# Optimization experiments

Hardware: AMD Instinct MI355X
Metric: run time of the kernel (lower is better)

## Reference

```python
import jax, jax.numpy as jnp
import numpy as np

KSIZE = 7
CUBIC_A = -0.5


def cubic_contribution(x, a=CUBIC_A):
    ax = jnp.abs(x)
    ax2 = ax * ax
    ax3 = ax * ax2
    cont_01 = ((a + 2) * ax3 - (a + 3) * ax2 + 1) * (ax <= 1).astype(x.dtype)
    cont_12 = (a * ax3 - 5 * a * ax2 + 8 * a * ax - 4 * a) * jnp.logical_and(ax > 1, ax <= 2).astype(x.dtype)
    return cont_01 + cont_12


def projective_grid(H, W, m, eps_x=0.0, eps_y=0.0):
    # Apply 3x3 homography m to pixel centers (x+eps_x, y+eps_y); returns (2, H*W).
    xs = jnp.arange(W, dtype=jnp.float32) + eps_x
    ys = jnp.arange(H, dtype=jnp.float32) + eps_y
    yy, xx = jnp.meshgrid(ys, xs, indexing='ij')
    xx = xx.ravel()
    yy = yy.ravel()
    X = m[0, 0] * xx + m[0, 1] * yy + m[0, 2]
    Y = m[1, 0] * xx + m[1, 1] * yy + m[1, 2]
    Z = m[2, 0] * xx + m[2, 1] * yy + m[2, 2]
    return jnp.stack((X / Z, Y / Z))


def setup_inputs() -> dict:
    key = jax.random.key(0)
    k1, k2 = jax.random.split(key)
    H = W = 1024
    N = H * W
    # near-identity homography (avoids degenerate perspective divide)
    m_inverse = jnp.eye(3, dtype=jnp.float32) + 0.001 * jax.random.normal(k1, (3, 3), dtype=jnp.float32)
    # source-space sampling positions, in-image range
    grid = jax.random.uniform(k2, (2, N), dtype=jnp.float32) * jnp.array([[W - 1.0], [H - 1.0]], dtype=jnp.float32)
    yi = jnp.arange(N, dtype=jnp.int32)
    return {"m_inverse": m_inverse, "grid": grid, "H": H, "W": W, "yi": yi}


def reference(m_inverse, grid, H, W, yi):
    K = KSIZE
    pad = K // 2
    offset = (K % 2) / 2  # 0.5 for odd kernels

    pos = grid + 1 - offset                      # (2, N)
    pos_frac = pos - jnp.floor(pos)              # (2, N)

    pl = projective_grid(H, W, m_inverse, eps_x=-0.5)
    pr = projective_grid(H, W, m_inverse, eps_x=0.5)
    pt = projective_grid(H, W, m_inverse, eps_y=-0.5)
    pb = projective_grid(H, W, m_inverse, eps_y=0.5)

    du = (pb - pt)[:, yi][:, :, None, None]      # (2, N, 1, 1)
    dv = (pr - pl)[:, yi][:, :, None, None]      # (2, N, 1, 1)

    # regularize |du| >= 1
    len_du = jnp.sqrt(du[0] ** 2 + du[1] ** 2)   # (N, 1, 1)
    mask_du = len_du < 1.0
    du = jnp.where(mask_du[None], du / len_du[None], du)
    len_du = jnp.where(mask_du, 1.0, len_du)

    # regularize |dv| >= 1
    len_dv = jnp.sqrt(dv[0] ** 2 + dv[1] ** 2)
    mask_dv = len_dv < 1.0
    dv = jnp.where(mask_dv[None], dv / len_dv[None], dv)
    len_dv = jnp.where(mask_dv, 1.0, len_dv)

    det = du[0] * dv[1] - du[1] * dv[0]          # (N, 1, 1)
    len_du = len_du * det
    len_dv = len_dv * det

    pos_w = jnp.linspace(pad - K + 1, pad, K).astype(jnp.float32) + offset  # (K,)
    pw = pos_frac[:, :, None] - pos_w[None, None, :]                        # (2, N, K)
    pos_wx = pw[0][:, None, :]                   # (N, 1, K)
    pos_wy = pw[1][:, :, None]                   # (N, K, 1)

    pos_wxp = (dv[1] * pos_wx - du[1] * pos_wy) / len_du  # (N, K, K)
    pos_wyp = (du[0] * pos_wy - dv[0] * pos_wx) / len_dv  # (N, K, K)

    x = du[0] * pos_wxp + du[1] * pos_wyp        # (N, K, K)
    y = dv[0] * pos_wxp + dv[1] * pos_wyp        # (N, K, K)

    weight = (cubic_contribution(x) * cubic_contribution(y)).reshape(x.shape[0], -1)  # (N, K*K)
    weight = weight / jnp.sum(weight, axis=-1, keepdims=True)
    return weight
```

## Files before the change

### kernel.cpp

```cpp
#include <hip/hip_runtime.h>

#define K 7
#define KK 49
#define BLK 256
#define TPP 2
#define PPB (BLK / TPP)
#define NW 25
#define CHUNK_F4 (PPB * KK / 4)

__device__ __forceinline__ float cubic_c(float x) {
    float ax = __builtin_fabsf(x);
    float t2 = __builtin_fmaxf(2.0f - ax, 0.0f);
    float t1 = __builtin_fmaxf(1.0f - ax, 0.0f);
    float r  = (t2 * t2) * __builtin_fmaf(0.5f, t2, -0.5f);
    return __builtin_fmaf(t1 * t1, __builtin_fmaf(-2.0f, t1, 1.0f), r);
}

__global__ __launch_bounds__(BLK, 6) void kest_kernel(
    const float* __restrict__ m,
    const float* __restrict__ grid,
    const int*   __restrict__ Wp,
    const int*   __restrict__ yi,
    float*       __restrict__ out,
    int N)
{
    __shared__ __align__(16) float lds[PPB * KK];

    const int tid  = threadIdx.x;
    const int sub  = tid & (TPP - 1);
    const int pixL = tid >> 1;
    const int i    = blockIdx.x * PPB + pixL;

    if (i < N) {
        const float m00 = m[0], m01 = m[1], m02 = m[2];
        const float m10 = m[3], m11 = m[4], m12 = m[5];
        const float m20 = m[6], m21 = m[7], m22 = m[8];
        const int   W   = Wp[0];

        const int j = yi[i];
        int yyI, xxI;
        if ((W & (W - 1)) == 0) {
            yyI = j >> (__ffs(W) - 1);
            xxI = j & (W - 1);
        } else {
            yyI = j / W;
            xxI = j - yyI * W;
        }
        const float xx = (float)xxI;
        const float yy = (float)yyI;

        const float X0 = m00 * xx + m01 * yy + m02;
        const float Y0 = m10 * xx + m11 * yy + m12;
        const float Z0 = m20 * xx + m21 * yy + m22;

        const float izy = __builtin_amdgcn_rcpf(Z0 * Z0 - 0.25f * m21 * m21);
        float du0 = (m01 * Z0 - m21 * X0) * izy;
        float du1 = (m11 * Z0 - m21 * Y0) * izy;
        const float izx = __builtin_amdgcn_rcpf(Z0 * Z0 - 0.25f * m20 * m20);
        float dv0 = (m00 * Z0 - m20 * X0) * izx;
        float dv1 = (m10 * Z0 - m20 * Y0) * izx;

        const float d2u = du0 * du0 + du1 * du1;
        const float rlu = __builtin_amdgcn_rsqf(d2u);
        float len_du = d2u * rlu;
        if (len_du < 1.0f) { du0 *= rlu; du1 *= rlu; len_du = 1.0f; }
        const float d2v = dv0 * dv0 + dv1 * dv1;
        const float rlv = __builtin_amdgcn_rsqf(d2v);
        float len_dv = d2v * rlv;
        if (len_dv < 1.0f) { dv0 *= rlv; dv1 *= rlv; len_dv = 1.0f; }

        const float det  = du0 * dv1 - du1 * dv0;
        const float r_du = __builtin_amdgcn_rcpf(len_du * det);
        const float r_dv = __builtin_amdgcn_rcpf(len_dv * det);

        const float p1 = du0 * dv1, p2 = du1 * dv0;
        const float Axx = p1 * r_du - p2 * r_dv;
        const float Axy = du0 * du1 * (r_dv - r_du);
        const float Ayx = dv0 * dv1 * (r_du - r_dv);
        const float Ayy = p1 * r_dv - p2 * r_du;

        const float px  = grid[i]     + 0.5f;
        const float py  = grid[N + i] + 0.5f;
        const float fxc = (px - __builtin_floorf(px)) + 2.5f;
        const float fyc = (py - __builtin_floorf(py)) + 2.5f;
        const float subf = (float)sub;

        float wv[NW];
        float wsum = 0.0f;
#pragma unroll
        for (int qq = 0; qq < NW; ++qq) {
            const int c0 = (2 * qq) % 7,  c1 = (2 * qq + 1) % 7;
            const int r0 = (2 * qq) / 7,  r1 = (2 * qq + 1) / 7;
            const float wxv = __builtin_fmaf(subf, (float)(c0 - c1), fxc - (float)c0);
            const float wyv = __builtin_fmaf(subf, (float)(r0 - r1), fyc - (float)r0);
            const float x = __builtin_fmaf(Axx, wxv, Axy * wyv);
            const float y = __builtin_fmaf(Ayx, wxv, Ayy * wyv);
            float t = cubic_c(x) * cubic_c(y);
            if (qq == NW - 1) t = sub ? 0.0f : t;
            wv[qq] = t;
            wsum += t;
        }
        wsum += __shfl_xor(wsum, 1);
        const float rs = __builtin_amdgcn_rcpf(wsum);

        float* p = &lds[pixL * KK + sub];
#pragma unroll
        for (int qq = 0; qq < NW; ++qq) {
            if (qq < NW - 1 || sub == 0)
                p[2 * qq] = wv[qq] * rs;
        }
    }
    __syncthreads();

    const long long baseF4 = (long long)blockIdx.x * CHUNK_F4;
    const long long limF4  = ((long long)N * KK) >> 2;
    const float4* src = (const float4*)lds;
    float4*       dst = (float4*)out + baseF4;
#pragma unroll
    for (int k = 0; k < 7; ++k) {
        const int t = tid + k * BLK;
        if (t < CHUNK_F4 && baseF4 + t < limF4) dst[t] = src[t];
    }
}

extern "C" void kernel_launch(void* const* d_in, const int* in_sizes, int n_in,
                              void* d_out, int out_size, void* d_ws, size_t ws_size,
                              hipStream_t stream) {
    const float* m    = (const float*)d_in[0];
    const float* grid = (const float*)d_in[1];
    const int*   Wp   = (const int*)d_in[3];
    const int*   yi   = (const int*)d_in[4];
    float*       out  = (float*)d_out;
    const int N = in_sizes[4];

    const int blocks = (N + PPB - 1) / PPB;
    kest_kernel<<<blocks, BLK, 0, stream>>>(m, grid, Wp, yi, out, N);
}
```

Baseline: 219.8 us.

## Share per-pixel setup via shuffles, use packed float2 math, per-wave LDS staging

Only the first 32 lanes of each wavefront compute the per-pixel homography Jacobian and fractional offsets. The results are broadcast with shuffles to the two threads that handle each pixel, so the setup work is no longer done twice. The 49-tap cubic weight loop is rewritten with two-wide float vectors so the compiler can emit packed FP32 instructions. Each wavefront now stages and stores its own LDS slice, which removes the block-wide barrier, and a scalar tail path handles the partial last block. The costs are extra shuffle instructions and a reliance on intra-wave ordering of LDS writes and reads without an explicit barrier.

```diff
diff --git a/kernel.cpp b/kernel.cpp
--- a/kernel.cpp
+++ b/kernel.cpp
@@ -1,19 +1,23 @@
 #include <hip/hip_runtime.h>
 
-#define K 7
 #define KK 49
 #define BLK 256
-#define TPP 2
-#define PPB (BLK / TPP)
-#define NW 25
-#define CHUNK_F4 (PPB * KK / 4)
+#define PPW 32
+#define PPB 128
+#define WFL (PPW * KK)
+#define WF4 (WFL / 4)
 
-__device__ __forceinline__ float cubic_c(float x) {
-    float ax = __builtin_fabsf(x);
-    float t2 = __builtin_fmaxf(2.0f - ax, 0.0f);
-    float t1 = __builtin_fmaxf(1.0f - ax, 0.0f);
-    float r  = (t2 * t2) * __builtin_fmaf(0.5f, t2, -0.5f);
-    return __builtin_fmaf(t1 * t1, __builtin_fmaf(-2.0f, t1, 1.0f), r);
+typedef float v2f __attribute__((ext_vector_type(2)));
+
+static __device__ __forceinline__ v2f v2bc(float s) { v2f r; r.x = s; r.y = s; return r; }
+
+static __device__ __forceinline__ v2f cubic2(v2f x) {
+    v2f ax = __builtin_elementwise_abs(x);
+    v2f t2 = __builtin_elementwise_max(v2bc(2.0f) - ax, v2bc(0.0f));
+    v2f t1 = __builtin_elementwise_max(v2bc(1.0f) - ax, v2bc(0.0f));
+    v2f r  = (t2 * t2) * __builtin_elementwise_fma(v2bc(0.5f), t2, v2bc(-0.5f));
+    return __builtin_elementwise_fma(t1 * t1,
+              __builtin_elementwise_fma(v2bc(-2.0f), t1, v2bc(1.0f)), r);
 }
 
 __global__ __launch_bounds__(BLK, 6) void kest_kernel(
@@ -24,102 +28,145 @@
     float*       __restrict__ out,
     int N)
 {
-    __shared__ __align__(16) float lds[PPB * KK];
+    __shared__ __align__(16) float lds[4 * WFL];
 
-    const int tid  = threadIdx.x;
-    const int sub  = tid & (TPP - 1);
-    const int pixL = tid >> 1;
-    const int i    = blockIdx.x * PPB + pixL;
+    const int tid   = threadIdx.x;
+    const int wv_   = tid >> 6;
+    const int lane  = tid & 63;
+    const int pixW  = lane >> 1;
+    const int sub   = lane & 1;
+    const int blockBase = blockIdx.x * PPB;
+    float* ldsW = &lds[wv_ * WFL];
 
+    float Axx = 0.f, Axy = 0.f, Ayx = 0.f, Ayy = 0.f, fxc = 0.f, fyc = 0.f;
+    if (lane < 32) {
+        const int p = blockBase + wv_ * PPW + lane;
+        if (p < N) {
+            const float m00 = m[0], m01 = m[1], m02 = m[2];
+            const float m10 = m[3], m11 = m[4], m12 = m[5];
+            const float m20 = m[6], m21 = m[7], m22 = m[8];
+            const int   W   = Wp[0];
+
+            const int j = yi[p];
+            int yyI, xxI;
+            if ((W & (W - 1)) == 0) {
+                yyI = j >> (__ffs(W) - 1);
+                xxI = j & (W - 1);
+            } else {
+                yyI = j / W;
+                xxI = j - yyI * W;
+            }
+            const float xx = (float)xxI, yy = (float)yyI;
+
+            const float X0 = m00 * xx + m01 * yy + m02;
+            const float Y0 = m10 * xx + m11 * yy + m12;
+            const float Z0 = m20 * xx + m21 * yy + m22;
+
+            const float izy = __builtin_amdgcn_rcpf(Z0 * Z0 - 0.25f * m21 * m21);
+            float du0 = (m01 * Z0 - m21 * X0) * izy;
+            float du1 = (m11 * Z0 - m21 * Y0) * izy;
+            const float izx = __builtin_amdgcn_rcpf(Z0 * Z0 - 0.25f * m20 * m20);
+            float dv0 = (m00 * Z0 - m20 * X0) * izx;
+            float dv1 = (m10 * Z0 - m20 * Y0) * izx;
+
+            const float d2u = du0 * du0 + du1 * du1;
+            const float rlu = __builtin_amdgcn_rsqf(d2u);
+            float len_du = d2u * rlu;
+            if (len_du < 1.0f) { du0 *= rlu; du1 *= rlu; len_du = 1.0f; }
+            const float d2v = dv0 * dv0 + dv1 * dv1;
+            const float rlv = __builtin_amdgcn_rsqf(d2v);
+            float len_dv = d2v * rlv;
+            if (len_dv < 1.0f) { dv0 *= rlv; dv1 *= rlv; len_dv = 1.0f; }
+
+            const float det  = du0 * dv1 - du1 * dv0;
+            const float r_du = __builtin_amdgcn_rcpf(len_du * det);
+            const float r_dv = __builtin_amdgcn_rcpf(len_dv * det);
+
+            const float p1 = du0 * dv1, p2 = du1 * dv0;
+            Axx = p1 * r_du - p2 * r_dv;
+            Axy = du0 * du1 * (r_dv - r_du);
+            Ayx = dv0 * dv1 * (r_du - r_dv);
+            Ayy = p1 * r_dv - p2 * r_du;
+
+            const float px = grid[p]     + 0.5f;
+            const float py = grid[N + p] + 0.5f;
+            fxc = (px - __builtin_floorf(px)) + 2.5f;
+            fyc = (py - __builtin_floorf(py)) + 2.5f;
+        }
+    }
+    Axx = __shfl(Axx, pixW); Axy = __shfl(Axy, pixW);
+    Ayx = __shfl(Ayx, pixW); Ayy = __shfl(Ayy, pixW);
+    fxc = __shfl(fxc, pixW); fyc = __shfl(fyc, pixW);
+
+    const int i = blockBase + wv_ * PPW + pixW;
     if (i < N) {
-        const float m00 = m[0], m01 = m[1], m02 = m[2];
-        const float m10 = m[3], m11 = m[4], m12 = m[5];
-        const float m20 = m[6], m21 = m[7], m22 = m[8];
-        const int   W   = Wp[0];
+        const float subf = (float)sub;
+        const v2f subf2 = v2bc(subf);
+        const v2f Axx2 = v2bc(Axx), Axy2 = v2bc(Axy);
+        const v2f Ayx2 = v2bc(Ayx), Ayy2 = v2bc(Ayy);
 
-        const int j = yi[i];
-        int yyI, xxI;
-        if ((W & (W - 1)) == 0) {
-            yyI = j >> (__ffs(W) - 1);
-            xxI = j & (W - 1);
-        } else {
-            yyI = j / W;
-            xxI = j - yyI * W;
+        v2f wv2[13];
+        v2f ws2 = v2bc(0.0f);
+#pragma unroll
+        for (int j = 0; j < 13; ++j) {
+            const int q0 = 4 * j, q1 = 4 * j + 2;
+            const float cx0 = (float)(q0 % 7), cx1 = (float)(q1 % 7);
+            const float dx0 = (float)((q0 + 1) % 7 - q0 % 7);
+            const float dx1 = (float)((q1 + 1) % 7 - q1 % 7);
+            const float ry0 = (float)(q0 / 7), ry1 = (float)(q1 / 7);
+            const float dy0 = (float)((q0 + 1) / 7 - q0 / 7);
+            const float dy1 = (float)((q1 + 1) / 7 - q1 / 7);
+
+            v2f wxv; wxv.x = fxc - cx0; wxv.y = fxc - cx1;
+            v2f dxv; dxv.x = -dx0;      dxv.y = -dx1;
+            wxv = __builtin_elementwise_fma(subf2, dxv, wxv);
+            v2f wyv; wyv.x = fyc - ry0; wyv.y = fyc - ry1;
+            v2f dyv; dyv.x = -dy0;      dyv.y = -dy1;
+            wyv = __builtin_elementwise_fma(subf2, dyv, wyv);
+
+            v2f x2 = __builtin_elementwise_fma(Axx2, wxv, Axy2 * wyv);
+            v2f y2 = __builtin_elementwise_fma(Ayx2, wxv, Ayy2 * wyv);
+            v2f w2 = cubic2(x2) * cubic2(y2);
+            if (j == 12) {
+                w2.x *= (1.0f - subf);
+                w2.y  = 0.0f;
+            }
+            ws2 += w2;
+            wv2[j] = w2;
         }
-        const float xx = (float)xxI;
-        const float yy = (float)yyI;
-
-        const float X0 = m00 * xx + m01 * yy + m02;
-        const float Y0 = m10 * xx + m11 * yy + m12;
-        const float Z0 = m20 * xx + m21 * yy + m22;
-
-        const float izy = __builtin_amdgcn_rcpf(Z0 * Z0 - 0.25f * m21 * m21);
-        float du0 = (m01 * Z0 - m21 * X0) * izy;
-        float du1 = (m11 * Z0 - m21 * Y0) * izy;
-        const float izx = __builtin_amdgcn_rcpf(Z0 * Z0 - 0.25f * m20 * m20);
-        float dv0 = (m00 * Z0 - m20 * X0) * izx;
-        float dv1 = (m10 * Z0 - m20 * Y0) * izx;
-
-        const float d2u = du0 * du0 + du1 * du1;
-        const float rlu = __builtin_amdgcn_rsqf(d2u);
-        float len_du = d2u * rlu;
-        if (len_du < 1.0f) { du0 *= rlu; du1 *= rlu; len_du = 1.0f; }
-        const float d2v = dv0 * dv0 + dv1 * dv1;
-        const float rlv = __builtin_amdgcn_rsqf(d2v);
-        float len_dv = d2v * rlv;
-        if (len_dv < 1.0f) { dv0 *= rlv; dv1 *= rlv; len_dv = 1.0f; }
-
-        const float det  = du0 * dv1 - du1 * dv0;
-        const float r_du = __builtin_amdgcn_rcpf(len_du * det);
-        const float r_dv = __builtin_amdgcn_rcpf(len_dv * det);
-
-        const float p1 = du0 * dv1, p2 = du1 * dv0;
-        const float Axx = p1 * r_du - p2 * r_dv;
-        const float Axy = du0 * du1 * (r_dv - r_du);
-        const float Ayx = dv0 * dv1 * (r_du - r_dv);
-        const float Ayy = p1 * r_dv - p2 * r_du;
-
-        const float px  = grid[i]     + 0.5f;
-        const float py  = grid[N + i] + 0.5f;
-        const float fxc = (px - __builtin_floorf(px)) + 2.5f;
-        const float fyc = (py - __builtin_floorf(py)) + 2.5f;
-        const float subf = (float)sub;
-
-        float wv[NW];
-        float wsum = 0.0f;
-#pragma unroll
-        for (int qq = 0; qq < NW; ++qq) {
-            const int c0 = (2 * qq) % 7,  c1 = (2 * qq + 1) % 7;
-            const int r0 = (2 * qq) / 7,  r1 = (2 * qq + 1) / 7;
-            const float wxv = __builtin_fmaf(subf, (float)(c0 - c1), fxc - (float)c0);
-            const float wyv = __builtin_fmaf(subf, (float)(r0 - r1), fyc - (float)r0);
-            const float x = __builtin_fmaf(Axx, wxv, Axy * wyv);
-            const float y = __builtin_fmaf(Ayx, wxv, Ayy * wyv);
-            float t = cubic_c(x) * cubic_c(y);
-            if (qq == NW - 1) t = sub ? 0.0f : t;
-            wv[qq] = t;
-            wsum += t;
-        }
+        float wsum = ws2.x + ws2.y;
         wsum += __shfl_xor(wsum, 1);
         const float rs = __builtin_amdgcn_rcpf(wsum);
+        const v2f rs2 = v2bc(rs);
 
-        float* p = &lds[pixL * KK + sub];
+        float* base = &ldsW[pixW * KK + sub];
 #pragma unroll
-        for (int qq = 0; qq < NW; ++qq) {
-            if (qq < NW - 1 || sub == 0)
-                p[2 * qq] = wv[qq] * rs;
+        for (int j = 0; j < 13; ++j) {
+            const v2f v = wv2[j] * rs2;
+            if (j < 12) {
+                base[4 * j]     = v.x;
+                base[4 * j + 2] = v.y;
+            } else if (sub == 0) {
+                base[48] = v.x;
+            }
         }
     }
-    __syncthreads();
 
-    const long long baseF4 = (long long)blockIdx.x * CHUNK_F4;
-    const long long limF4  = ((long long)N * KK) >> 2;
-    const float4* src = (const float4*)lds;
-    float4*       dst = (float4*)out + baseF4;
+    const long long dstF4 = (long long)blockIdx.x * (PPB * KK / 4) + wv_ * WF4;
+    if (blockBase + PPB <= N) {
+        const float4* src = (const float4*)ldsW;
+        float4* dst = (float4*)out + dstF4;
 #pragma unroll
-    for (int k = 0; k < 7; ++k) {
-        const int t = tid + k * BLK;
-        if (t < CHUNK_F4 && baseF4 + t < limF4) dst[t] = src[t];
+        for (int k = 0; k < 7; ++k) {
+            const int t = lane + 64 * k;
+            if (t < WF4) dst[t] = src[t];
+        }
+    } else {
+        const float* s = (const float*)ldsW;
+        const long long baseF = dstF4 * 4;
+        const long long limF  = (long long)N * KK;
+        for (int t = lane; t < WFL; t += 64)
+            if (baseF + t < limF) out[baseF + t] = s[t];
     }
 }
 
```

After: 217.7 us. Within noise of the previous version (-1.0%).
